# Performance work log

Measured on AMD Instinct MI355X. Metric: run time of the kernel, lower is better.

The kernel has to match this reference:

```python
import jax, jax.numpy as jnp
import numpy as np

N_HEAD, D_MODEL, D_K, D_V = 8, 512, 64, 64
B, S = 4, 2048
LN_EPS = 1e-5


def setup_inputs() -> dict:
    key = jax.random.key(0)
    ks = jax.random.split(key, 12)
    std_qk = np.sqrt(2.0 / (D_MODEL + D_K))
    std_v = np.sqrt(2.0 / (D_MODEL + D_V))
    return {
        "q": jax.random.normal(ks[0], (B, S, D_MODEL), jnp.float32),
        "k": jax.random.normal(ks[1], (B, S, D_MODEL), jnp.float32),
        "v": jax.random.normal(ks[2], (B, S, D_MODEL), jnp.float32),
        "w_qs": jax.random.normal(ks[3], (N_HEAD * D_K, D_MODEL), jnp.float32) * std_qk,
        "b_qs": jnp.zeros((N_HEAD * D_K,), jnp.float32),
        "w_ks": jax.random.normal(ks[4], (N_HEAD * D_K, D_MODEL), jnp.float32) * std_qk,
        "b_ks": jnp.zeros((N_HEAD * D_K,), jnp.float32),
        "w_vs": jax.random.normal(ks[5], (N_HEAD * D_V, D_MODEL), jnp.float32) * std_v,
        "b_vs": jnp.zeros((N_HEAD * D_V,), jnp.float32),
        "w_fc": jax.random.normal(ks[6], (D_MODEL, N_HEAD * D_V), jnp.float32) * np.sqrt(2.0 / (D_MODEL + N_HEAD * D_V)),
        "b_fc": jnp.zeros((D_MODEL,), jnp.float32),
        "ln_g": jnp.ones((D_MODEL,), jnp.float32),
        "ln_b": jnp.zeros((D_MODEL,), jnp.float32),
    }


def reference(q, k, v, w_qs, b_qs, w_ks, b_ks, w_vs, b_vs, w_fc, b_fc, ln_g, ln_b):
    sz_b, len_q, _ = q.shape
    residual = q
    temperature = np.power(D_K, 0.5).astype(np.float32)
    # Projections: [b, s, h*dk] -> [h, b, s, dk]  (matches permute(2,0,1,3))
    qh = (jnp.einsum('bsd,fd->bsf', q, w_qs) + b_qs).reshape(sz_b, len_q, N_HEAD, D_K).transpose(2, 0, 1, 3)
    kh = (jnp.einsum('bsd,fd->bsf', k, w_ks) + b_ks).reshape(sz_b, -1, N_HEAD, D_K).transpose(2, 0, 1, 3)
    vh = (jnp.einsum('bsd,fd->bsf', v, w_vs) + b_vs).reshape(sz_b, -1, N_HEAD, D_V).transpose(2, 0, 1, 3)
    # Scaled dot-product attention (dropout is identity in eval)
    attn = jnp.einsum('hbqd,hbkd->hbqk', qh, kh) / temperature
    attn = jax.nn.softmax(attn, axis=-1)
    out = jnp.einsum('hbqk,hbkv->hbqv', attn, vh)          # [h, b, q, dv]
    out = out.transpose(1, 2, 0, 3).reshape(sz_b, len_q, N_HEAD * D_V)
    out = jnp.einsum('bsf,df->bsd', out, w_fc) + b_fc
    # Residual + LayerNorm
    x = out + residual
    mu = jnp.mean(x, axis=-1, keepdims=True)
    var = jnp.mean(jnp.square(x - mu), axis=-1, keepdims=True)
    x = (x - mu) * jax.lax.rsqrt(var + LN_EPS) * ln_g + ln_b
    # attn returned as [(n_head*b), len_q, len_k] to match torch bmm layout
    return x, attn.reshape(N_HEAD * sz_b, len_q, -1)
```

## Files before the change

### kernel.cpp

```cpp
#include <hip/hip_runtime.h>
#include <hip/hip_bf16.h>

constexpr int NB  = 4;
constexpr int NS  = 2048;
constexpr int NH  = 8;
constexpr int DM  = 512;
constexpr int DKV = 64;
constexpr int HB  = NH * NB;

typedef __attribute__((ext_vector_type(8))) short short8;
typedef __attribute__((ext_vector_type(4))) float f32x4;

__device__ inline unsigned short f2bf(float f) {
    unsigned u = __builtin_bit_cast(unsigned, f);
    u = (u + 0x7fffu + ((u >> 16) & 1u)) >> 16;
    return (unsigned short)u;
}
__device__ inline float bf2f(unsigned short h) {
    unsigned u = ((unsigned)h) << 16;
    return __builtin_bit_cast(float, u);
}
__device__ inline short8 ld8(const unsigned short* p) { return *(const short8*)p; }

__device__ inline short8 pack8(const float* p) {
    f32x4 a = *(const f32x4*)p;
    f32x4 b = *(const f32x4*)(p + 4);
    short8 r;
    r[0] = (short)f2bf(a[0]); r[1] = (short)f2bf(a[1]);
    r[2] = (short)f2bf(a[2]); r[3] = (short)f2bf(a[3]);
    r[4] = (short)f2bf(b[0]); r[5] = (short)f2bf(b[1]);
    r[6] = (short)f2bf(b[2]); r[7] = (short)f2bf(b[3]);
    return r;
}

__device__ inline f32x4 mfma16(short8 a, short8 b, f32x4 c) {
    return __builtin_amdgcn_mfma_f32_16x16x32_bf16(a, b, c, 0, 0, 0);
}

__device__ inline void gl_lds16(const void* g, void* l) {
    __builtin_amdgcn_global_load_lds(
        (const __attribute__((address_space(1))) unsigned*)g,
        (__attribute__((address_space(3))) unsigned*)l, 16, 0, 0);
}

__global__ __launch_bounds__(256) void k_cvtw(const float* __restrict__ s0,
                                              const float* __restrict__ s1,
                                              const float* __restrict__ s2,
                                              const float* __restrict__ s3,
                                              unsigned short* __restrict__ d0,
                                              unsigned short* __restrict__ d1,
                                              unsigned short* __restrict__ d2,
                                              unsigned short* __restrict__ d3)
{
    const float* s; unsigned short* d;
    switch (blockIdx.y) {
        case 0:  s = s0; d = d0; break;
        case 1:  s = s1; d = d1; break;
        case 2:  s = s2; d = d2; break;
        default: s = s3; d = d3; break;
    }
    const size_t i = ((size_t)blockIdx.x * 256 + threadIdx.x) * 8;
    *(short8*)(d + i) = pack8(s + i);
}

__global__ __launch_bounds__(256) void k_cvtx(const float* __restrict__ s0,
                                              const float* __restrict__ s1,
                                              const float* __restrict__ s2,
                                              unsigned short* __restrict__ d0,
                                              unsigned short* __restrict__ d1,
                                              unsigned short* __restrict__ d2)
{
    const float* s; unsigned short* d;
    switch (blockIdx.y) {
        case 0:  s = s0; d = d0; break;
        case 1:  s = s1; d = d1; break;
        default: s = s2; d = d2; break;
    }
    const size_t i = ((size_t)blockIdx.x * 256 + threadIdx.x) * 8;
    *(short8*)(d + i) = pack8(s + i);
}

__global__ __launch_bounds__(256, 4) void k_proj(const unsigned short* __restrict__ X,
                                              const unsigned short* __restrict__ W,
                                              const float* __restrict__ bias,
                                              unsigned short* __restrict__ out,
                                              float scale, int vtrans)
{
    const int tid = threadIdx.x;
    const int l = tid & 63, w = tid >> 6;
    const int c = l & 15, g = l >> 4;
    const int m0 = blockIdx.y * 64 + w * 16;
    const int f0 = blockIdx.x * 64;
    const int arow = m0 + c;

    f32x4 acc[4] = {};
    const unsigned short* aB = X + (size_t)arow * DM;
    for (int kb = 0; kb < DM; kb += 32) {
        short8 af = ld8(aB + kb + g * 8);
#pragma unroll
        for (int n = 0; n < 4; ++n) {
            short8 bf = ld8(W + (size_t)(f0 + n * 16 + c) * DM + kb + g * 8);
            acc[n] = mfma16(af, bf, acc[n]);
        }
    }
#pragma unroll
    for (int n = 0; n < 4; ++n) {
        const int f = f0 + n * 16 + c;
        const int h = f >> 6, d = f & 63;
        const float bv = bias[f];
#pragma unroll
        for (int r = 0; r < 4; ++r) {
            const int m = m0 + g * 4 + r;
            const int bb = m >> 11, s = m & (NS - 1);
            const int hb = h * NB + bb;
            const float v = (acc[n][r] + bv) * scale;
            const size_t idx = vtrans ? ((size_t)(hb * DKV + d) * NS + s)
                                      : ((size_t)(hb * NS + s) * DKV + d);
            out[idx] = f2bf(v);
        }
    }
}

__global__ __launch_bounds__(256, 4) void k_attn(const unsigned short* __restrict__ Qh,
                                                 const unsigned short* __restrict__ Kh,
                                                 const unsigned short* __restrict__ Vt,
                                                 float* __restrict__ attn,
                                                 unsigned short* __restrict__ Obuf)
{
    __shared__ __align__(16) char kld[8192];
    __shared__ __align__(16) char vld[8192];
    __shared__ __align__(16) char plds[4 * 2048];
    const int tid = threadIdx.x;
    const int l = tid & 63, w = tid >> 6;
    const int c = l & 15, g = l >> 4;

    const int bid = blockIdx.x;
    const int wid = (bid & 7) * 128 + (bid >> 3);
    const int hb = wid >> 5;
    const int q0 = (wid & 31) * 64 + w * 16;
    char* myp = plds + w * 2048;

    const char* kbytes = (const char*)(Kh + (size_t)hb * NS * DKV);
    const char* vbytes = (const char*)(Vt + (size_t)hb * DKV * NS);

    const unsigned short* qb = Qh + ((size_t)hb * NS + q0 + c) * DKV + g * 8;
    const short8 qf0 = ld8(qb), qf1 = ld8(qb + 32);

    int koff[2], voff[2];
#pragma unroll
    for (int j = 0; j < 2; ++j) {
        const int D = (w * 2 + j) * 1024 + l * 16;
        const int row = D >> 7;
        const int scolb = (D & 127) ^ ((row & 7) << 4);
        koff[j] = row * 128 + scolb;
        voff[j] = row * (NS * 2) + scolb;
    }
    const int swc = (c & 7) << 4;

    float ls[4] = {0.f, 0.f, 0.f, 0.f};
    for (int kt = 0; kt < NS / 64; ++kt) {
        const size_t k0b = (size_t)kt * 64 * 128;
        __syncthreads();
        gl_lds16(kbytes + k0b + koff[0], kld + (w * 2 + 0) * 1024);
        gl_lds16(kbytes + k0b + koff[1], kld + (w * 2 + 1) * 1024);
        __syncthreads();
#pragma unroll
        for (int t = 0; t < 4; ++t) {
            const int rb = (t * 16 + c) * 128;
            const short8 b0 = *(const short8*)(kld + rb + ((g * 16) ^ swc));
            const short8 b1 = *(const short8*)(kld + rb + ((64 + g * 16) ^ swc));
            f32x4 z = {};
            z = mfma16(qf0, b0, z);
            z = mfma16(qf1, b1, z);
#pragma unroll
            for (int r = 0; r < 4; ++r) ls[r] += exp2f(z[r]);
        }
    }
    float li[4];
#pragma unroll
    for (int r = 0; r < 4; ++r) {
        float s = ls[r];
        s += __shfl_xor(s, 1);
        s += __shfl_xor(s, 2);
        s += __shfl_xor(s, 4);
        s += __shfl_xor(s, 8);
        li[r] = 1.0f / s;
    }

    f32x4 oacc[4] = {};
    const int srow = l >> 2, sseg = l & 3;
    float* srowp = attn + (size_t)hb * NS * NS + (size_t)(q0 + srow) * NS + sseg * 16;
    const int swsr = (srow & 7) << 4;

    for (int kt = 0; kt < NS / 64; ++kt) {
        const int k0 = kt * 64;
        const size_t k0b = (size_t)k0 * 128;
        __syncthreads();
        gl_lds16(kbytes + k0b + koff[0], kld + (w * 2 + 0) * 1024);
        gl_lds16(kbytes + k0b + koff[1], kld + (w * 2 + 1) * 1024);
        gl_lds16(vbytes + (size_t)k0 * 2 + voff[0], vld + (w * 2 + 0) * 1024);
        gl_lds16(vbytes + (size_t)k0 * 2 + voff[1], vld + (w * 2 + 1) * 1024);
        __syncthreads();
        f32x4 sc[4];
#pragma unroll
        for (int t = 0; t < 4; ++t) {
            const int rb = (t * 16 + c) * 128;
            const short8 b0 = *(const short8*)(kld + rb + ((g * 16) ^ swc));
            const short8 b1 = *(const short8*)(kld + rb + ((64 + g * 16) ^ swc));
            f32x4 z = {};
            z = mfma16(qf0, b0, z);
            z = mfma16(qf1, b1, z);
            sc[t] = z;
        }
#pragma unroll
        for (int t = 0; t < 4; ++t)
#pragma unroll
            for (int r = 0; r < 4; ++r) {
                const float p = exp2f(sc[t][r]) * li[r];
                const int row = g * 4 + r;
                int by = row * 128 + (t * 16 + c) * 2;
                by ^= (row & 7) << 4;
                *(unsigned short*)(myp + by) = f2bf(p);
            }
        asm volatile("s_waitcnt lgkmcnt(0)" ::: "memory");
        __builtin_amdgcn_sched_barrier(0);
#pragma unroll
        for (int kk = 0; kk < 2; ++kk) {
            const short8 pa = *(const short8*)(myp + c * 128 + ((kk * 64 + g * 16) ^ swc));
#pragma unroll
            for (int n = 0; n < 4; ++n) {
                const int rb = (n * 16 + c) * 128;
                const short8 vb = *(const short8*)(vld + rb + ((kk * 64 + g * 16) ^ swc));
                oacc[n] = mfma16(pa, vb, oacc[n]);
            }
        }
        {
            const short8 p0 = *(const short8*)(myp + srow * 128 + ((sseg * 32) ^ swsr));
            const short8 p1 = *(const short8*)(myp + srow * 128 + ((sseg * 32 + 16) ^ swsr));
            f32x4 o0, o1, o2, o3;
#pragma unroll
            for (int j = 0; j < 4; ++j) {
                o0[j] = bf2f((unsigned short)p0[j]);
                o1[j] = bf2f((unsigned short)p0[4 + j]);
                o2[j] = bf2f((unsigned short)p1[j]);
                o3[j] = bf2f((unsigned short)p1[4 + j]);
            }
            float* dst = srowp + k0;
            *(f32x4*)(dst)      = o0;
            *(f32x4*)(dst + 4)  = o1;
            *(f32x4*)(dst + 8)  = o2;
            *(f32x4*)(dst + 12) = o3;
        }
    }

    const int h = hb >> 2, bb = hb & 3;
#pragma unroll
    for (int n = 0; n < 4; ++n)
#pragma unroll
        for (int r = 0; r < 4; ++r) {
            const int q = q0 + g * 4 + r;
            const int dv = n * 16 + c;
            Obuf[((size_t)(bb * NS + q)) * DM + h * DKV + dv] = f2bf(oacc[n][r]);
        }
}

__global__ __launch_bounds__(256, 4) void k_fc(const unsigned short* __restrict__ O,
                                            const unsigned short* __restrict__ Wfc,
                                            const float* __restrict__ bfc,
                                            const float* __restrict__ resid,
                                            unsigned short* __restrict__ Y)
{
    const int tid = threadIdx.x;
    const int l = tid & 63, w = tid >> 6;
    const int c = l & 15, g = l >> 4;
    const int m0 = blockIdx.y * 64 + w * 16;
    const int f0 = blockIdx.x * 64;
    const int arow = m0 + c;

    f32x4 acc[4] = {};
    const unsigned short* aB = O + (size_t)arow * DM;
    for (int kb = 0; kb < DM; kb += 32) {
        short8 af = ld8(aB + kb + g * 8);
#pragma unroll
        for (int n = 0; n < 4; ++n) {
            short8 bf = ld8(Wfc + (size_t)(f0 + n * 16 + c) * DM + kb + g * 8);
            acc[n] = mfma16(af, bf, acc[n]);
        }
    }
#pragma unroll
    for (int n = 0; n < 4; ++n) {
        const int d = f0 + n * 16 + c;
        const float bv = bfc[d];
#pragma unroll
        for (int r = 0; r < 4; ++r) {
            const int m = m0 + g * 4 + r;
            const float v = acc[n][r] + bv + resid[(size_t)m * DM + d];
            Y[(size_t)m * DM + d] = f2bf(v);
        }
    }
}

__global__ __launch_bounds__(256) void k_ln(const unsigned short* __restrict__ Y,
                                            const float* __restrict__ gam,
                                            const float* __restrict__ bet,
                                            float* __restrict__ out)
{
    const int tid = threadIdx.x;
    const int l = tid & 63, w = tid >> 6;
    const int row = blockIdx.x * 4 + w;

    const short8 yv = ld8(Y + (size_t)row * DM + l * 8);
    float x[8];
#pragma unroll
    for (int j = 0; j < 8; ++j) x[j] = bf2f((unsigned short)yv[j]);

    float s = 0.f;
#pragma unroll
    for (int j = 0; j < 8; ++j) s += x[j];
#pragma unroll
    for (int mask = 1; mask <= 32; mask <<= 1) s += __shfl_xor(s, mask);
    const float mean = s * (1.0f / DM);

    float d2 = 0.f;
#pragma unroll
    for (int j = 0; j < 8; ++j) { const float t = x[j] - mean; d2 += t * t; }
#pragma unroll
    for (int mask = 1; mask <= 32; mask <<= 1) d2 += __shfl_xor(d2, mask);
    const float rstd = rsqrtf(d2 * (1.0f / DM) + 1e-5f);

#pragma unroll
    for (int j = 0; j < 8; ++j) {
        const int d = l * 8 + j;
        out[(size_t)row * DM + d] = (x[j] - mean) * rstd * gam[d] + bet[d];
    }
}

extern "C" void kernel_launch(void* const* d_in, const int* in_sizes, int n_in,
                              void* d_out, int out_size, void* d_ws, size_t ws_size,
                              hipStream_t stream)
{
    const float* q    = (const float*)d_in[0];
    const float* k    = (const float*)d_in[1];
    const float* v    = (const float*)d_in[2];
    const float* w_qs = (const float*)d_in[3];
    const float* b_qs = (const float*)d_in[4];
    const float* w_ks = (const float*)d_in[5];
    const float* b_ks = (const float*)d_in[6];
    const float* w_vs = (const float*)d_in[7];
    const float* b_vs = (const float*)d_in[8];
    const float* w_fc = (const float*)d_in[9];
    const float* b_fc = (const float*)d_in[10];
    const float* ln_g = (const float*)d_in[11];
    const float* ln_b = (const float*)d_in[12];

    char* ws = (char*)d_ws;
    unsigned short* Qh = (unsigned short*)(ws);
    unsigned short* Kh = (unsigned short*)(ws + (8u  << 20));
    unsigned short* Vt = (unsigned short*)(ws + (16u << 20));
    unsigned short* Ob = (unsigned short*)(ws + (24u << 20));
    unsigned short* Yb = (unsigned short*)(ws + (32u << 20));
    unsigned short* Wq = (unsigned short*)(ws + (40u << 20));
    unsigned short* Wk = Wq + (size_t)DM * DM;
    unsigned short* Wv = Wk + (size_t)DM * DM;
    unsigned short* Wf = Wv + (size_t)DM * DM;
    unsigned short* Xq = (unsigned short*)(ws + (48u << 20));
    unsigned short* Xk = (unsigned short*)(ws + (56u << 20));
    unsigned short* Xv = (unsigned short*)(ws + (64u << 20));

    float* xout = (float*)d_out;
    float* attn = xout + (size_t)NB * NS * DM;

    k_cvtw<<<dim3(128, 4), 256, 0, stream>>>(w_qs, w_ks, w_vs, w_fc, Wq, Wk, Wv, Wf);
    k_cvtx<<<dim3(2048, 3), 256, 0, stream>>>(q, k, v, Xq, Xk, Xv);

    const float qscale = 0.125f * 1.44269504088896340736f;
    const dim3 gproj(8, 128);
    k_proj<<<gproj, 256, 0, stream>>>(Xq, Wq, b_qs, Qh, qscale, 0);
    k_proj<<<gproj, 256, 0, stream>>>(Xk, Wk, b_ks, Kh, 1.0f, 0);
    k_proj<<<gproj, 256, 0, stream>>>(Xv, Wv, b_vs, Vt, 1.0f, 1);

    k_attn<<<1024, 256, 0, stream>>>(Qh, Kh, Vt, attn, Ob);

    k_fc<<<gproj, 256, 0, stream>>>(Ob, Wf, b_fc, q, Yb);
    k_ln<<<NB * NS / 4, 256, 0, stream>>>(Yb, ln_g, ln_b, xout);
}
```

Before: 440.4 us.

## Double-buffer K/V LDS tiles in attention and merge conversion kernels

Both attention passes now prefetch the next K (and V) tile into a second LDS buffer with direct global-to-LDS loads while the current tile is computed. This replaces the two __syncthreads per iteration with one barrier plus vmcnt waits. The large fp32 attention-probability writes become nontemporal stores and are issued before the PV MFMAs. The weight and activation fp32-to-bf16 conversion kernels are merged into one launch. LDS use per block goes up from 24KB to 40KB, which may limit occupancy.

New measurement: 866.0 us. 1.97x slower.

```diff
diff --git a/kernel.cpp b/kernel.cpp
--- a/kernel.cpp
+++ b/kernel.cpp
@@ -43,40 +43,41 @@
         (__attribute__((address_space(3))) unsigned*)l, 16, 0, 0);
 }
 
-__global__ __launch_bounds__(256) void k_cvtw(const float* __restrict__ s0,
-                                              const float* __restrict__ s1,
-                                              const float* __restrict__ s2,
-                                              const float* __restrict__ s3,
-                                              unsigned short* __restrict__ d0,
-                                              unsigned short* __restrict__ d1,
-                                              unsigned short* __restrict__ d2,
-                                              unsigned short* __restrict__ d3)
-{
-    const float* s; unsigned short* d;
-    switch (blockIdx.y) {
-        case 0:  s = s0; d = d0; break;
-        case 1:  s = s1; d = d1; break;
-        case 2:  s = s2; d = d2; break;
-        default: s = s3; d = d3; break;
-    }
-    const size_t i = ((size_t)blockIdx.x * 256 + threadIdx.x) * 8;
-    *(short8*)(d + i) = pack8(s + i);
-}
-
-__global__ __launch_bounds__(256) void k_cvtx(const float* __restrict__ s0,
-                                              const float* __restrict__ s1,
-                                              const float* __restrict__ s2,
-                                              unsigned short* __restrict__ d0,
-                                              unsigned short* __restrict__ d1,
-                                              unsigned short* __restrict__ d2)
-{
-    const float* s; unsigned short* d;
-    switch (blockIdx.y) {
-        case 0:  s = s0; d = d0; break;
-        case 1:  s = s1; d = d1; break;
-        default: s = s2; d = d2; break;
-    }
-    const size_t i = ((size_t)blockIdx.x * 256 + threadIdx.x) * 8;
+__device__ inline void bar() { __builtin_amdgcn_s_barrier(); }
+
+__global__ __launch_bounds__(256) void k_cvt(const float* __restrict__ x0,
+                                             const float* __restrict__ x1,
+                                             const float* __restrict__ x2,
+                                             const float* __restrict__ w0,
+                                             const float* __restrict__ w1,
+                                             const float* __restrict__ w2,
+                                             const float* __restrict__ w3,
+                                             unsigned short* __restrict__ dx0,
+                                             unsigned short* __restrict__ dx1,
+                                             unsigned short* __restrict__ dx2,
+                                             unsigned short* __restrict__ dw0,
+                                             unsigned short* __restrict__ dw1,
+                                             unsigned short* __restrict__ dw2,
+                                             unsigned short* __restrict__ dw3)
+{
+    const float* s; unsigned short* d; size_t i;
+    if (blockIdx.y < 3) {
+        switch (blockIdx.y) {
+            case 0:  s = x0; d = dx0; break;
+            case 1:  s = x1; d = dx1; break;
+            default: s = x2; d = dx2; break;
+        }
+        i = ((size_t)blockIdx.x * 256 + threadIdx.x) * 8;
+    } else {
+        if (blockIdx.x >= 512) return;
+        switch (blockIdx.x >> 7) {
+            case 0:  s = w0; d = dw0; break;
+            case 1:  s = w1; d = dw1; break;
+            case 2:  s = w2; d = dw2; break;
+            default: s = w3; d = dw3; break;
+        }
+        i = ((size_t)(blockIdx.x & 127) * 256 + threadIdx.x) * 8;
+    }
     *(short8*)(d + i) = pack8(s + i);
 }
 
@@ -127,8 +128,8 @@
                                                  float* __restrict__ attn,
                                                  unsigned short* __restrict__ Obuf)
 {
-    __shared__ __align__(16) char kld[8192];
-    __shared__ __align__(16) char vld[8192];
+    __shared__ __align__(16) char kld[2][8192];
+    __shared__ __align__(16) char vld[2][8192];
     __shared__ __align__(16) char plds[4 * 2048];
     const int tid = threadIdx.x;
     const int l = tid & 63, w = tid >> 6;
@@ -157,23 +158,36 @@
     }
     const int swc = (c & 7) << 4;
 
+    const int ldsbase = w * 2048;
+
     float ls[4] = {0.f, 0.f, 0.f, 0.f};
-    for (int kt = 0; kt < NS / 64; ++kt) {
-        const size_t k0b = (size_t)kt * 64 * 128;
-        __syncthreads();
-        gl_lds16(kbytes + k0b + koff[0], kld + (w * 2 + 0) * 1024);
-        gl_lds16(kbytes + k0b + koff[1], kld + (w * 2 + 1) * 1024);
-        __syncthreads();
-#pragma unroll
-        for (int t = 0; t < 4; ++t) {
-            const int rb = (t * 16 + c) * 128;
-            const short8 b0 = *(const short8*)(kld + rb + ((g * 16) ^ swc));
-            const short8 b1 = *(const short8*)(kld + rb + ((64 + g * 16) ^ swc));
-            f32x4 z = {};
-            z = mfma16(qf0, b0, z);
-            z = mfma16(qf1, b1, z);
-#pragma unroll
-            for (int r = 0; r < 4; ++r) ls[r] += exp2f(z[r]);
+    {
+        gl_lds16(kbytes + koff[0], kld[0] + ldsbase);
+        gl_lds16(kbytes + koff[1], kld[0] + ldsbase + 1024);
+        asm volatile("s_waitcnt vmcnt(0)" ::: "memory");
+        bar();
+        int cur = 0;
+        for (int kt = 0; kt < NS / 64; ++kt) {
+            if (kt + 1 < NS / 64) {
+                const size_t nb = (size_t)(kt + 1) * 64 * 128;
+                gl_lds16(kbytes + nb + koff[0], kld[cur ^ 1] + ldsbase);
+                gl_lds16(kbytes + nb + koff[1], kld[cur ^ 1] + ldsbase + 1024);
+                asm volatile("s_waitcnt vmcnt(2)" ::: "memory");
+            }
+            __builtin_amdgcn_sched_barrier(0);
+#pragma unroll
+            for (int t = 0; t < 4; ++t) {
+                const int rb = (t * 16 + c) * 128;
+                const short8 b0 = *(const short8*)(kld[cur] + rb + ((g * 16) ^ swc));
+                const short8 b1 = *(const short8*)(kld[cur] + rb + ((64 + g * 16) ^ swc));
+                f32x4 z = {};
+                z = mfma16(qf0, b0, z);
+                z = mfma16(qf1, b1, z);
+#pragma unroll
+                for (int r = 0; r < 4; ++r) ls[r] += exp2f(z[r]);
+            }
+            bar();
+            cur ^= 1;
         }
     }
     float li[4];
@@ -192,64 +206,80 @@
     float* srowp = attn + (size_t)hb * NS * NS + (size_t)(q0 + srow) * NS + sseg * 16;
     const int swsr = (srow & 7) << 4;
 
-    for (int kt = 0; kt < NS / 64; ++kt) {
-        const int k0 = kt * 64;
-        const size_t k0b = (size_t)k0 * 128;
-        __syncthreads();
-        gl_lds16(kbytes + k0b + koff[0], kld + (w * 2 + 0) * 1024);
-        gl_lds16(kbytes + k0b + koff[1], kld + (w * 2 + 1) * 1024);
-        gl_lds16(vbytes + (size_t)k0 * 2 + voff[0], vld + (w * 2 + 0) * 1024);
-        gl_lds16(vbytes + (size_t)k0 * 2 + voff[1], vld + (w * 2 + 1) * 1024);
-        __syncthreads();
-        f32x4 sc[4];
-#pragma unroll
-        for (int t = 0; t < 4; ++t) {
-            const int rb = (t * 16 + c) * 128;
-            const short8 b0 = *(const short8*)(kld + rb + ((g * 16) ^ swc));
-            const short8 b1 = *(const short8*)(kld + rb + ((64 + g * 16) ^ swc));
-            f32x4 z = {};
-            z = mfma16(qf0, b0, z);
-            z = mfma16(qf1, b1, z);
-            sc[t] = z;
-        }
-#pragma unroll
-        for (int t = 0; t < 4; ++t)
-#pragma unroll
-            for (int r = 0; r < 4; ++r) {
-                const float p = exp2f(sc[t][r]) * li[r];
-                const int row = g * 4 + r;
-                int by = row * 128 + (t * 16 + c) * 2;
-                by ^= (row & 7) << 4;
-                *(unsigned short*)(myp + by) = f2bf(p);
-            }
-        asm volatile("s_waitcnt lgkmcnt(0)" ::: "memory");
-        __builtin_amdgcn_sched_barrier(0);
-#pragma unroll
-        for (int kk = 0; kk < 2; ++kk) {
-            const short8 pa = *(const short8*)(myp + c * 128 + ((kk * 64 + g * 16) ^ swc));
-#pragma unroll
-            for (int n = 0; n < 4; ++n) {
-                const int rb = (n * 16 + c) * 128;
-                const short8 vb = *(const short8*)(vld + rb + ((kk * 64 + g * 16) ^ swc));
-                oacc[n] = mfma16(pa, vb, oacc[n]);
-            }
-        }
-        {
-            const short8 p0 = *(const short8*)(myp + srow * 128 + ((sseg * 32) ^ swsr));
-            const short8 p1 = *(const short8*)(myp + srow * 128 + ((sseg * 32 + 16) ^ swsr));
-            f32x4 o0, o1, o2, o3;
-#pragma unroll
-            for (int j = 0; j < 4; ++j) {
-                o0[j] = bf2f((unsigned short)p0[j]);
-                o1[j] = bf2f((unsigned short)p0[4 + j]);
-                o2[j] = bf2f((unsigned short)p1[j]);
-                o3[j] = bf2f((unsigned short)p1[4 + j]);
-            }
-            float* dst = srowp + k0;
-            *(f32x4*)(dst)      = o0;
-            *(f32x4*)(dst + 4)  = o1;
-            *(f32x4*)(dst + 8)  = o2;
-            *(f32x4*)(dst + 12) = o3;
+    {
+        gl_lds16(kbytes + koff[0], kld[0] + ldsbase);
+        gl_lds16(kbytes + koff[1], kld[0] + ldsbase + 1024);
+        gl_lds16(vbytes + voff[0], vld[0] + ldsbase);
+        gl_lds16(vbytes + voff[1], vld[0] + ldsbase + 1024);
+        asm volatile("s_waitcnt vmcnt(0)" ::: "memory");
+        bar();
+        int cur = 0;
+        for (int kt = 0; kt < NS / 64; ++kt) {
+            const int k0 = kt * 64;
+            if (kt + 1 < NS / 64) {
+                const size_t nkb = (size_t)(k0 + 64) * 128;
+                const size_t nvb = (size_t)(k0 + 64) * 2;
+                gl_lds16(kbytes + nkb + koff[0], kld[cur ^ 1] + ldsbase);
+                gl_lds16(kbytes + nkb + koff[1], kld[cur ^ 1] + ldsbase + 1024);
+                gl_lds16(vbytes + nvb + voff[0], vld[cur ^ 1] + ldsbase);
+                gl_lds16(vbytes + nvb + voff[1], vld[cur ^ 1] + ldsbase + 1024);
+                asm volatile("s_waitcnt vmcnt(4)" ::: "memory");
+            } else {
+                asm volatile("s_waitcnt vmcnt(0)" ::: "memory");
+            }
+            __builtin_amdgcn_sched_barrier(0);
+            f32x4 sc[4];
+#pragma unroll
+            for (int t = 0; t < 4; ++t) {
+                const int rb = (t * 16 + c) * 128;
+                const short8 b0 = *(const short8*)(kld[cur] + rb + ((g * 16) ^ swc));
+                const short8 b1 = *(const short8*)(kld[cur] + rb + ((64 + g * 16) ^ swc));
+                f32x4 z = {};
+                z = mfma16(qf0, b0, z);
+                z = mfma16(qf1, b1, z);
+                sc[t] = z;
+            }
+#pragma unroll
+            for (int t = 0; t < 4; ++t)
+#pragma unroll
+                for (int r = 0; r < 4; ++r) {
+                    const float p = exp2f(sc[t][r]) * li[r];
+                    const int row = g * 4 + r;
+                    int by = row * 128 + (t * 16 + c) * 2;
+                    by ^= (row & 7) << 4;
+                    *(unsigned short*)(myp + by) = f2bf(p);
+                }
+            asm volatile("s_waitcnt lgkmcnt(0)" ::: "memory");
+            __builtin_amdgcn_sched_barrier(0);
+            {
+                const short8 p0 = *(const short8*)(myp + srow * 128 + ((sseg * 32) ^ swsr));
+                const short8 p1 = *(const short8*)(myp + srow * 128 + ((sseg * 32 + 16) ^ swsr));
+                f32x4 o0, o1, o2, o3;
+#pragma unroll
+                for (int j = 0; j < 4; ++j) {
+                    o0[j] = bf2f((unsigned short)p0[j]);
+                    o1[j] = bf2f((unsigned short)p0[4 + j]);
+                    o2[j] = bf2f((unsigned short)p1[j]);
+                    o3[j] = bf2f((unsigned short)p1[4 + j]);
+                }
+                float* dst = srowp + k0;
+                __builtin_nontemporal_store(o0, (f32x4*)(dst));
+                __builtin_nontemporal_store(o1, (f32x4*)(dst + 4));
+                __builtin_nontemporal_store(o2, (f32x4*)(dst + 8));
+                __builtin_nontemporal_store(o3, (f32x4*)(dst + 12));
+            }
+#pragma unroll
+            for (int kk = 0; kk < 2; ++kk) {
+                const short8 pa = *(const short8*)(myp + c * 128 + ((kk * 64 + g * 16) ^ swc));
+#pragma unroll
+                for (int n = 0; n < 4; ++n) {
+                    const int rb = (n * 16 + c) * 128;
+                    const short8 vb = *(const short8*)(vld[cur] + rb + ((kk * 64 + g * 16) ^ swc));
+                    oacc[n] = mfma16(pa, vb, oacc[n]);
+                }
+            }
+            bar();
+            cur ^= 1;
         }
     }
 
@@ -370,8 +400,8 @@
     float* xout = (float*)d_out;
     float* attn = xout + (size_t)NB * NS * DM;
 
-    k_cvtw<<<dim3(128, 4), 256, 0, stream>>>(w_qs, w_ks, w_vs, w_fc, Wq, Wk, Wv, Wf);
-    k_cvtx<<<dim3(2048, 3), 256, 0, stream>>>(q, k, v, Xq, Xk, Xv);
+    k_cvt<<<dim3(2048, 4), 256, 0, stream>>>(q, k, v, w_qs, w_ks, w_vs, w_fc,
+                                             Xq, Xk, Xv, Wq, Wk, Wv, Wf);
 
     const float qscale = 0.125f * 1.44269504088896340736f;
     const dim3 gproj(8, 128);
```
